# Optimization experiments

Hardware: AMD Instinct MI355X
Metric: run time of the kernel (lower is better)

The kernel has to match this reference:

```python
import jax, jax.numpy as jnp
import numpy as np

DIM = 512
NUM_HEADS = 4  # min(4, 512 // 16)
HEAD_DIM = DIM // NUM_HEADS  # 128


def setup_inputs() -> dict:
    key = jax.random.key(0)
    ks = jax.random.split(key, 5)
    B, N = 2, 4096
    s = DIM ** -0.5
    return {
        "x": jax.random.normal(ks[0], (B, N, DIM), dtype=jnp.float32),
        "qkv_w": jax.random.normal(ks[1], (3 * DIM, DIM), dtype=jnp.float32) * s,
        "qkv_b": jax.random.normal(ks[2], (3 * DIM,), dtype=jnp.float32) * 0.02,
        "proj_w": jax.random.normal(ks[3], (DIM, DIM), dtype=jnp.float32) * s,
        "proj_b": jax.random.normal(ks[4], (DIM,), dtype=jnp.float32) * 0.02,
    }


def reference(x, qkv_w, qkv_b, proj_w, proj_b):
    B, N, C = x.shape
    H, D = NUM_HEADS, HEAD_DIM
    # torch Linear: x @ W^T + b
    qkv = x @ qkv_w.T + qkv_b                      # [B, N, 3C]
    qkv = qkv.reshape(B, N, 3, H, D)
    q = qkv[:, :, 0].transpose(0, 2, 1, 3)         # [B, H, N, D]
    k = qkv[:, :, 1].transpose(0, 2, 1, 3)
    v = qkv[:, :, 2].transpose(0, 2, 1, 3)
    scale = D ** -0.5
    attn = jnp.einsum('bhnd,bhmd->bhnm', q, k) * scale  # [B, H, N, N]
    attn = jax.nn.softmax(attn, axis=-1)
    # dropout(p=0.1) is identity in eval mode
    out = jnp.einsum('bhnm,bhmd->bhnd', attn, v)   # [B, H, N, D]
    out = out.transpose(0, 2, 1, 3).reshape(B, N, C)
    return out @ proj_w.T + proj_b
```

## Files before the change

### kernel.cpp

```cpp
#include <hip/hip_runtime.h>
#include <hip/hip_bf16.h>
#include <stdint.h>

constexpr int B_  = 2;
constexpr int N_  = 4096;
constexpr int C_  = 512;
constexpr int H_  = 4;
constexpr int D_  = 128;
constexpr int M_  = B_ * N_;
constexpr int TC_ = 3 * C_;
constexpr float SCALE_  = 0.08838834764831845f;
constexpr float LOG2E_  = 1.4426950408889634f;
constexpr float KSCALE_ = SCALE_ * LOG2E_;

typedef __attribute__((ext_vector_type(8))) short short8;
typedef __attribute__((ext_vector_type(4))) float f32x4;

#define GLOBAL_AS __attribute__((address_space(1)))
#define LDS_AS    __attribute__((address_space(3)))

static __device__ __forceinline__ void load_lds16(const void* gp, void* lp) {
    __builtin_amdgcn_global_load_lds((const GLOBAL_AS void*)gp, (LDS_AS void*)lp,
                                     16, 0, 0);
}

static __device__ __forceinline__ uint16_t f2bf(float f) {
    uint32_t u = __builtin_bit_cast(uint32_t, f);
    uint32_t r = (u + 0x7FFFu + ((u >> 16) & 1u)) >> 16;
    return (uint16_t)r;
}
static __device__ __forceinline__ uint32_t cvt_pk_bf16(float lo, float hi) {
    uint32_t r;
    asm("v_cvt_pk_bf16_f32 %0, %1, %2" : "=v"(r) : "v"(lo), "v"(hi));
    return r;
}
static __device__ __forceinline__ float exp2f_fast(float x) {
    float r;
    asm("v_exp_f32 %0, %1" : "=v"(r) : "v"(x));
    return r;
}

__global__ __launch_bounds__(256)
void cast3_kernel(const float* __restrict__ x,  const float* __restrict__ w,
                  const float* __restrict__ pw,
                  uint16_t* __restrict__ xb, uint16_t* __restrict__ wb,
                  uint16_t* __restrict__ pwb)
{
    const int bid = blockIdx.x;
    const float* src; uint16_t* dst; int i;
    if (bid < 2048)      { src = x;  dst = xb;  i = bid * 256 + threadIdx.x; }
    else if (bid < 2432) { src = w;  dst = wb;  i = (bid - 2048) * 256 + threadIdx.x; }
    else                 { src = pw; dst = pwb; i = (bid - 2432) * 256 + threadIdx.x; }
    float4 a = reinterpret_cast<const float4*>(src)[2*i];
    float4 b = reinterpret_cast<const float4*>(src)[2*i+1];
    uint4 o;
    o.x = (uint32_t)f2bf(a.x) | ((uint32_t)f2bf(a.y) << 16);
    o.y = (uint32_t)f2bf(a.z) | ((uint32_t)f2bf(a.w) << 16);
    o.z = (uint32_t)f2bf(b.x) | ((uint32_t)f2bf(b.y) << 16);
    o.w = (uint32_t)f2bf(b.z) | ((uint32_t)f2bf(b.w) << 16);
    reinterpret_cast<uint4*>(dst)[i] = o;
}

__global__ __launch_bounds__(256, 2)
void gemm_qkv(const uint16_t* __restrict__ A,
              const uint16_t* __restrict__ Bw,
              const float* __restrict__ bias,
              uint16_t* __restrict__ Qb,
              uint16_t* __restrict__ Kb,
              uint16_t* __restrict__ Vt)
{
    __shared__ __align__(16) uint16_t SMEM[128 * 128];
    uint16_t* As = SMEM;
    uint16_t* Bs = SMEM + 128 * 64;

    const int tid  = threadIdx.x;
    const int lane = tid & 63;
    const int w    = tid >> 6;
    const int wr   = w >> 1, wc = w & 1;
    const int cq   = lane & 15;
    const int g    = lane >> 4;
    const int m0   = blockIdx.x * 128;
    const int o0   = blockIdx.y * 128;

    f32x4 acc[4][4];
    const f32x4 zf = {0.f, 0.f, 0.f, 0.f};
    #pragma unroll
    for (int i = 0; i < 4; ++i)
        #pragma unroll
        for (int j = 0; j < 4; ++j) acc[i][j] = zf;

    for (int kt = 0; kt < C_; kt += 64) {
        __syncthreads();
        #pragma unroll
        for (int i = 0; i < 4; ++i) {
            int s = tid + 256 * i;
            int row = s >> 3, p = s & 7, c = p ^ (row & 7);
            load_lds16(A  + (size_t)(m0 + row) * C_ + kt + c * 8, &As[row*64 + p*8]);
            load_lds16(Bw + (size_t)(o0 + row) * C_ + kt + c * 8, &Bs[row*64 + p*8]);
        }
        __syncthreads();
        #pragma unroll
        for (int ks = 0; ks < 2; ++ks) {
            short8 af[4], bfr[4];
            #pragma unroll
            for (int mi = 0; mi < 4; ++mi) {
                int r = 64*wr + 16*mi + cq;
                af[mi] = *reinterpret_cast<const short8*>(
                    &As[r*64 + (((g + 4*ks) ^ (r & 7)) * 8)]);
            }
            #pragma unroll
            for (int ni = 0; ni < 4; ++ni) {
                int r = 64*wc + 16*ni + cq;
                bfr[ni] = *reinterpret_cast<const short8*>(
                    &Bs[r*64 + (((g + 4*ks) ^ (r & 7)) * 8)]);
            }
            #pragma unroll
            for (int mi = 0; mi < 4; ++mi)
                #pragma unroll
                for (int ni = 0; ni < 4; ++ni)
                    acc[mi][ni] = __builtin_amdgcn_mfma_f32_16x16x32_bf16(
                        af[mi], bfr[ni], acc[mi][ni], 0, 0, 0);
        }
    }

    const int sec = o0 >> 9;
    const int h   = (o0 >> 7) & 3;
    if (sec < 2) {
        #pragma unroll
        for (int ni = 0; ni < 4; ++ni) {
            const int o = o0 + 64*wc + 16*ni + cq;
            const int d = o & 127;
            const float bv = bias[o];
            #pragma unroll
            for (int mi = 0; mi < 4; ++mi) {
                #pragma unroll
                for (int r = 0; r < 4; ++r) {
                    const int m = m0 + 64*wr + 16*mi + 4*g + r;
                    const int b = m >> 12;
                    const int n = m & (N_ - 1);
                    const float y = acc[mi][ni][r] + bv;
                    if (sec == 0)
                        Qb[(((size_t)b*H_ + h)*N_ + n)*D_ + d] = f2bf(y);
                    else
                        Kb[(((size_t)b*H_ + h)*N_ + n)*D_ + d] = f2bf(y * KSCALE_);
                }
            }
        }
    } else {
        __syncthreads();
        uint16_t* T = SMEM;
        #pragma unroll
        for (int ni = 0; ni < 4; ++ni) {
            const int ol = 64*wc + 16*ni + cq;
            const float bv = bias[o0 + ol];
            #pragma unroll
            for (int mi = 0; mi < 4; ++mi) {
                const int ml = 64*wr + 16*mi + 4*g;
                const uint32_t w0 = (uint32_t)f2bf(acc[mi][ni][0] + bv)
                                  | ((uint32_t)f2bf(acc[mi][ni][1] + bv) << 16);
                const uint32_t w1 = (uint32_t)f2bf(acc[mi][ni][2] + bv)
                                  | ((uint32_t)f2bf(acc[mi][ni][3] + bv) << 16);
                *reinterpret_cast<uint2*>(&T[ol*128 + ml]) = make_uint2(w0, w1);
            }
        }
        __syncthreads();
        const int b = m0 >> 12;
        #pragma unroll
        for (int i = 0; i < 8; ++i) {
            int s = tid + 256 * i;
            int ro = s >> 4, mc = s & 15;
            int4 v = *reinterpret_cast<const int4*>(&T[ro*128 + mc*8]);
            const int n = (m0 & (N_ - 1)) + mc*8;
            *reinterpret_cast<int4*>(
                &Vt[(((size_t)b*H_ + h)*D_ + ro)*N_ + n]) = v;
        }
    }
}

__global__ __launch_bounds__(512, 1)
void attn_kernel(const uint16_t* __restrict__ Qb,
                 const uint16_t* __restrict__ Kb,
                 const uint16_t* __restrict__ Vt,
                 uint16_t* __restrict__ ctx)
{
    __shared__ __align__(16) uint16_t Ks[2][128 * 128];
    __shared__ __align__(16) uint16_t Vs[2][128 * 128];
    __shared__ __align__(16) uint16_t Ps[8][16 * 80];

    const int tid  = threadIdx.x;
    const int lane = tid & 63;
    const int w    = tid >> 6;
    const int qb   = w & 3;
    const int kvh  = w >> 2;
    const int cq   = lane & 15;
    const int g    = lane >> 4;

    const int bid = blockIdx.x;
    const int bh  = bid & 7;
    const int qt  = bid >> 3;
    const int b   = bh >> 2, h = bh & 3;

    const uint16_t* Qg = Qb + ((size_t)bh * N_ + qt * 128 + qb * 32) * D_;
    const uint16_t* Kg = Kb + (size_t)bh * N_ * D_;
    const uint16_t* Vg = Vt + (size_t)bh * D_ * N_;

    auto stage = [&](int tn, int bb) {
        const int kv0 = tn * 128;
        #pragma unroll
        for (int i = 0; i < 4; ++i) {
            int s = tid + 512 * i;
            int row = s >> 4, p = s & 15, c = p ^ (row & 15);
            load_lds16(Kg + (size_t)(kv0 + row) * D_ + c * 8,
                       &Ks[bb][row * 128 + p * 8]);
        }
        #pragma unroll
        for (int i = 0; i < 4; ++i) {
            int s = tid + 512 * i;
            int row = s >> 4, p = s & 15, c = p ^ (row & 15);
            load_lds16(Vg + (size_t)row * N_ + kv0 + c * 8,
                       &Vs[bb][row * 128 + p * 8]);
        }
    };

    stage(0, 0);

    short8 qreg[2][4];
    #pragma unroll
    for (int qf = 0; qf < 2; ++qf) {
        const uint16_t* qrow = Qg + (size_t)(16 * qf + cq) * D_;
        #pragma unroll
        for (int ks = 0; ks < 4; ++ks)
            qreg[qf][ks] = *reinterpret_cast<const short8*>(qrow + 32*ks + 8*g);
    }

    float m_run[2] = {-3.0e38f, -3.0e38f};
    float l_run[2] = {0.f, 0.f};
    f32x4 o_acc[8][2];
    const f32x4 zf = {0.f, 0.f, 0.f, 0.f};
    #pragma unroll
    for (int df = 0; df < 8; ++df) { o_acc[df][0] = zf; o_acc[df][1] = zf; }

    __syncthreads();

    for (int t = 0; t < N_ / 128; ++t) {
        const int cur = t & 1;
        if (t + 1 < N_ / 128) stage(t + 1, cur ^ 1);

        f32x4 sacc[4][2];
        #pragma unroll
        for (int kvf = 0; kvf < 4; ++kvf) { sacc[kvf][0] = zf; sacc[kvf][1] = zf; }
        #pragma unroll
        for (int ks = 0; ks < 4; ++ks) {
            #pragma unroll
            for (int kvf = 0; kvf < 4; ++kvf) {
                const int row = kvh*64 + 16*kvf + cq;
                const short8 ak = *reinterpret_cast<const short8*>(
                    &Ks[cur][row * 128 + (((g + 4*ks) ^ (row & 15)) * 8)]);
                sacc[kvf][0] = __builtin_amdgcn_mfma_f32_16x16x32_bf16(
                    ak, qreg[0][ks], sacc[kvf][0], 0, 0, 0);
                sacc[kvf][1] = __builtin_amdgcn_mfma_f32_16x16x32_bf16(
                    ak, qreg[1][ks], sacc[kvf][1], 0, 0, 0);
            }
        }

        short8 bp[2][2];
        #pragma unroll
        for (int qf = 0; qf < 2; ++qf) {
            float pmax = -3.0e38f;
            #pragma unroll
            for (int kvf = 0; kvf < 4; ++kvf)
                #pragma unroll
                for (int r = 0; r < 4; ++r)
                    pmax = fmaxf(pmax, sacc[kvf][qf][r]);
            pmax = fmaxf(pmax, __shfl_xor(pmax, 16));
            pmax = fmaxf(pmax, __shfl_xor(pmax, 32));

            if (__any(pmax > m_run[qf] + 8.f)) {
                const float mnew = fmaxf(m_run[qf], pmax);
                const float corr = exp2f_fast(m_run[qf] - mnew);
                m_run[qf] = mnew;
                l_run[qf] *= corr;
                #pragma unroll
                for (int df = 0; df < 8; ++df)
                    #pragma unroll
                    for (int r = 0; r < 4; ++r)
                        o_acc[df][qf][r] *= corr;
            }

            float lsum = 0.f;
            #pragma unroll
            for (int kvf = 0; kvf < 4; ++kvf) {
                const float p0 = exp2f_fast(sacc[kvf][qf][0] - m_run[qf]);
                const float p1 = exp2f_fast(sacc[kvf][qf][1] - m_run[qf]);
                const float p2 = exp2f_fast(sacc[kvf][qf][2] - m_run[qf]);
                const float p3 = exp2f_fast(sacc[kvf][qf][3] - m_run[qf]);
                lsum += (p0 + p1) + (p2 + p3);
                *reinterpret_cast<uint2*>(&Ps[w][cq*80 + 16*kvf + 4*g]) =
                    make_uint2(cvt_pk_bf16(p0, p1), cvt_pk_bf16(p2, p3));
            }
            lsum += __shfl_xor(lsum, 16);
            lsum += __shfl_xor(lsum, 32);
            l_run[qf] += lsum;

            #pragma unroll
            for (int ks = 0; ks < 2; ++ks)
                bp[qf][ks] = *reinterpret_cast<const short8*>(
                    &Ps[w][cq*80 + (4*ks + g) * 8]);
        }

        #pragma unroll
        for (int ks = 0; ks < 2; ++ks) {
            #pragma unroll
            for (int df = 0; df < 8; ++df) {
                const int row = 16*df + cq;
                const int ch  = kvh*8 + 4*ks + g;
                const short8 av = *reinterpret_cast<const short8*>(
                    &Vs[cur][row * 128 + ((ch ^ (row & 15)) * 8)]);
                o_acc[df][0] = __builtin_amdgcn_mfma_f32_16x16x32_bf16(
                    av, bp[0][ks], o_acc[df][0], 0, 0, 0);
                o_acc[df][1] = __builtin_amdgcn_mfma_f32_16x16x32_bf16(
                    av, bp[1][ks], o_acc[df][1], 0, 0, 0);
            }
        }
        __syncthreads();
    }

    float* mbuf = reinterpret_cast<float*>(&Ks[0][0]);
    float* lbuf = mbuf + 256;
    f32x4* obuf = reinterpret_cast<f32x4*>(&Vs[0][0]);

    if (kvh == 1) {
        #pragma unroll
        for (int qf = 0; qf < 2; ++qf) {
            mbuf[(qb*2 + qf)*16 + cq] = m_run[qf];
            lbuf[(qb*2 + qf)*16 + cq] = l_run[qf];
        }
        #pragma unroll
        for (int df = 0; df < 8; ++df)
            #pragma unroll
            for (int qf = 0; qf < 2; ++qf)
                obuf[qb*1024 + (df*2 + qf)*64 + lane] = o_acc[df][qf];
    }
    __syncthreads();
    if (kvh == 0) {
        #pragma unroll
        for (int qf = 0; qf < 2; ++qf) {
            const float mB = mbuf[(qb*2 + qf)*16 + cq];
            const float lB = lbuf[(qb*2 + qf)*16 + cq];
            const float ms = fmaxf(m_run[qf], mB);
            const float cA = exp2f_fast(m_run[qf] - ms);
            const float cB = exp2f_fast(mB - ms);
            const float inv = 1.f / (l_run[qf] * cA + lB * cB);

            const int n = qt*128 + qb*32 + 16*qf + cq;
            uint16_t* dst = ctx + ((size_t)b * N_ + n) * C_ + h * D_;
            #pragma unroll
            for (int df = 0; df < 8; ++df) {
                const f32x4 oB = obuf[qb*1024 + (df*2 + qf)*64 + lane];
                float v0 = (o_acc[df][qf][0]*cA + oB[0]*cB) * inv;
                float v1 = (o_acc[df][qf][1]*cA + oB[1]*cB) * inv;
                float v2 = (o_acc[df][qf][2]*cA + oB[2]*cB) * inv;
                float v3 = (o_acc[df][qf][3]*cA + oB[3]*cB) * inv;
                const uint32_t w0 = (uint32_t)f2bf(v0) | ((uint32_t)f2bf(v1) << 16);
                const uint32_t w1 = (uint32_t)f2bf(v2) | ((uint32_t)f2bf(v3) << 16);
                *reinterpret_cast<uint2*>(&dst[16*df + 4*g]) = make_uint2(w0, w1);
            }
        }
    }
}

__global__ __launch_bounds__(256, 2)
void gemm_proj(const uint16_t* __restrict__ A,
               const uint16_t* __restrict__ Bw,
               const float* __restrict__ bias,
               float* __restrict__ out)
{
    __shared__ __align__(16) uint16_t As[128 * 64];
    __shared__ __align__(16) uint16_t Bs[128 * 64];

    const int tid  = threadIdx.x;
    const int lane = tid & 63;
    const int w    = tid >> 6;
    const int wr   = w >> 1, wc = w & 1;
    const int cq   = lane & 15;
    const int g    = lane >> 4;
    const int m0   = blockIdx.x * 128;
    const int o0   = blockIdx.y * 128;

    f32x4 acc[4][4];
    const f32x4 zf = {0.f, 0.f, 0.f, 0.f};
    #pragma unroll
    for (int i = 0; i < 4; ++i)
        #pragma unroll
        for (int j = 0; j < 4; ++j) acc[i][j] = zf;

    for (int kt = 0; kt < C_; kt += 64) {
        __syncthreads();
        #pragma unroll
        for (int i = 0; i < 4; ++i) {
            int s = tid + 256 * i;
            int row = s >> 3, p = s & 7, c = p ^ (row & 7);
            load_lds16(A  + (size_t)(m0 + row) * C_ + kt + c * 8, &As[row*64 + p*8]);
            load_lds16(Bw + (size_t)(o0 + row) * C_ + kt + c * 8, &Bs[row*64 + p*8]);
        }
        __syncthreads();
        #pragma unroll
        for (int ks = 0; ks < 2; ++ks) {
            short8 af[4], bfr[4];
            #pragma unroll
            for (int mi = 0; mi < 4; ++mi) {
                int r = 64*wr + 16*mi + cq;
                af[mi] = *reinterpret_cast<const short8*>(
                    &As[r*64 + (((g + 4*ks) ^ (r & 7)) * 8)]);
            }
            #pragma unroll
            for (int ni = 0; ni < 4; ++ni) {
                int r = 64*wc + 16*ni + cq;
                bfr[ni] = *reinterpret_cast<const short8*>(
                    &Bs[r*64 + (((g + 4*ks) ^ (r & 7)) * 8)]);
            }
            #pragma unroll
            for (int mi = 0; mi < 4; ++mi)
                #pragma unroll
                for (int ni = 0; ni < 4; ++ni)
                    acc[mi][ni] = __builtin_amdgcn_mfma_f32_16x16x32_bf16(
                        af[mi], bfr[ni], acc[mi][ni], 0, 0, 0);
        }
    }

    #pragma unroll
    for (int ni = 0; ni < 4; ++ni) {
        const int o = o0 + 64*wc + 16*ni + cq;
        const float bv = bias[o];
        #pragma unroll
        for (int mi = 0; mi < 4; ++mi) {
            #pragma unroll
            for (int r = 0; r < 4; ++r) {
                const int m = m0 + 64*wr + 16*mi + 4*g + r;
                out[(size_t)m * C_ + o] = acc[mi][ni][r] + bv;
            }
        }
    }
}

extern "C" void kernel_launch(void* const* d_in, const int* in_sizes, int n_in,
                              void* d_out, int out_size, void* d_ws, size_t ws_size,
                              hipStream_t stream)
{
    const float* x      = (const float*)d_in[0];
    const float* qkv_w  = (const float*)d_in[1];
    const float* qkv_b  = (const float*)d_in[2];
    const float* proj_w = (const float*)d_in[3];
    const float* proj_b = (const float*)d_in[4];
    float* out = (float*)d_out;

    uint16_t* xb  = (uint16_t*)d_ws;
    uint16_t* wb  = xb  + (size_t)M_ * C_;
    uint16_t* pwb = wb  + (size_t)TC_ * C_;
    uint16_t* Qb  = pwb + (size_t)C_ * C_;
    uint16_t* Kb  = Qb  + (size_t)B_ * H_ * N_ * D_;
    uint16_t* Vt  = Kb  + (size_t)B_ * H_ * N_ * D_;
    uint16_t* ctx = Vt  + (size_t)B_ * H_ * N_ * D_;

    cast3_kernel<<<2560, 256, 0, stream>>>(x, qkv_w, proj_w, xb, wb, pwb);
    gemm_qkv<<<dim3(M_/128, TC_/128), 256, 0, stream>>>(xb, wb, qkv_b, Qb, Kb, Vt);
    attn_kernel<<<(N_/128) * (B_*H_), 512, 0, stream>>>(Qb, Kb, Vt, ctx);
    gemm_proj<<<dim3(M_/128, C_/128), 256, 0, stream>>>(ctx, pwb, proj_b, out);
}
```

Measured before the change: 196.0 us.

## Halve attention tile sizes to raise occupancy and flatten GEMM grids

The attention kernel now processes 64 queries per block (16 per wave) and 64-key tiles instead of 128, which halves LDS use and per-wave accumulator registers and raises the launch bound to 4 blocks per CU. The grid doubles to 512 blocks, giving more parallelism across CUs, and the P and V LDS swizzles are reworked for the narrower tiles. The QKV and projection GEMMs switch to a 1D grid with explicit tile decoding. The trade-off is less Q reuse of each K/V tile, so twice the K/V traffic per query and more loop iterations with barrier overhead.

```diff
diff --git a/kernel.cpp b/kernel.cpp
--- a/kernel.cpp
+++ b/kernel.cpp
@@ -79,8 +79,9 @@
     const int wr   = w >> 1, wc = w & 1;
     const int cq   = lane & 15;
     const int g    = lane >> 4;
-    const int m0   = blockIdx.x * 128;
-    const int o0   = blockIdx.y * 128;
+    const int bid  = blockIdx.x;
+    const int m0   = (bid & 63) << 7;
+    const int o0   = (bid >> 6) << 7;
 
     f32x4 acc[4][4];
     const f32x4 zf = {0.f, 0.f, 0.f, 0.f};
@@ -177,15 +178,15 @@
     }
 }
 
-__global__ __launch_bounds__(512, 1)
+__global__ __launch_bounds__(512, 4)
 void attn_kernel(const uint16_t* __restrict__ Qb,
                  const uint16_t* __restrict__ Kb,
                  const uint16_t* __restrict__ Vt,
                  uint16_t* __restrict__ ctx)
 {
-    __shared__ __align__(16) uint16_t Ks[2][128 * 128];
-    __shared__ __align__(16) uint16_t Vs[2][128 * 128];
-    __shared__ __align__(16) uint16_t Ps[8][16 * 80];
+    __shared__ __align__(16) uint16_t Ks[2][64 * 128];
+    __shared__ __align__(16) uint16_t Vs[2][128 * 64];
+    __shared__ __align__(16) uint16_t Ps[8 * 512];
 
     const int tid  = threadIdx.x;
     const int lane = tid & 63;
@@ -200,171 +201,148 @@
     const int qt  = bid >> 3;
     const int b   = bh >> 2, h = bh & 3;
 
-    const uint16_t* Qg = Qb + ((size_t)bh * N_ + qt * 128 + qb * 32) * D_;
+    const uint16_t* Qg = Qb + ((size_t)bh * N_ + qt * 64 + qb * 16) * D_;
     const uint16_t* Kg = Kb + (size_t)bh * N_ * D_;
     const uint16_t* Vg = Vt + (size_t)bh * D_ * N_;
 
     auto stage = [&](int tn, int bb) {
-        const int kv0 = tn * 128;
-        #pragma unroll
-        for (int i = 0; i < 4; ++i) {
+        const int kv0 = tn * 64;
+        #pragma unroll
+        for (int i = 0; i < 2; ++i) {
             int s = tid + 512 * i;
             int row = s >> 4, p = s & 15, c = p ^ (row & 15);
             load_lds16(Kg + (size_t)(kv0 + row) * D_ + c * 8,
                        &Ks[bb][row * 128 + p * 8]);
         }
         #pragma unroll
-        for (int i = 0; i < 4; ++i) {
+        for (int i = 0; i < 2; ++i) {
             int s = tid + 512 * i;
-            int row = s >> 4, p = s & 15, c = p ^ (row & 15);
+            int row = s >> 3, p = s & 7, c = p ^ (row & 7);
             load_lds16(Vg + (size_t)row * N_ + kv0 + c * 8,
-                       &Vs[bb][row * 128 + p * 8]);
+                       &Vs[bb][row * 64 + p * 8]);
         }
     };
 
     stage(0, 0);
 
-    short8 qreg[2][4];
-    #pragma unroll
-    for (int qf = 0; qf < 2; ++qf) {
-        const uint16_t* qrow = Qg + (size_t)(16 * qf + cq) * D_;
+    short8 qreg[4];
+    {
+        const uint16_t* qrow = Qg + (size_t)cq * D_;
         #pragma unroll
         for (int ks = 0; ks < 4; ++ks)
-            qreg[qf][ks] = *reinterpret_cast<const short8*>(qrow + 32*ks + 8*g);
-    }
-
-    float m_run[2] = {-3.0e38f, -3.0e38f};
-    float l_run[2] = {0.f, 0.f};
-    f32x4 o_acc[8][2];
+            qreg[ks] = *reinterpret_cast<const short8*>(qrow + 32*ks + 8*g);
+    }
+
+    float m_run = -3.0e38f, l_run = 0.f;
+    f32x4 o_acc[8];
     const f32x4 zf = {0.f, 0.f, 0.f, 0.f};
     #pragma unroll
-    for (int df = 0; df < 8; ++df) { o_acc[df][0] = zf; o_acc[df][1] = zf; }
+    for (int df = 0; df < 8; ++df) o_acc[df] = zf;
 
     __syncthreads();
 
-    for (int t = 0; t < N_ / 128; ++t) {
+    for (int t = 0; t < N_ / 64; ++t) {
         const int cur = t & 1;
-        if (t + 1 < N_ / 128) stage(t + 1, cur ^ 1);
-
-        f32x4 sacc[4][2];
-        #pragma unroll
-        for (int kvf = 0; kvf < 4; ++kvf) { sacc[kvf][0] = zf; sacc[kvf][1] = zf; }
+        if (t + 1 < N_ / 64) stage(t + 1, cur ^ 1);
+
+        f32x4 sacc[2];
+        sacc[0] = zf; sacc[1] = zf;
         #pragma unroll
         for (int ks = 0; ks < 4; ++ks) {
             #pragma unroll
-            for (int kvf = 0; kvf < 4; ++kvf) {
-                const int row = kvh*64 + 16*kvf + cq;
+            for (int kvf = 0; kvf < 2; ++kvf) {
+                const int row = kvh*32 + 16*kvf + cq;
                 const short8 ak = *reinterpret_cast<const short8*>(
-                    &Ks[cur][row * 128 + (((g + 4*ks) ^ (row & 15)) * 8)]);
-                sacc[kvf][0] = __builtin_amdgcn_mfma_f32_16x16x32_bf16(
-                    ak, qreg[0][ks], sacc[kvf][0], 0, 0, 0);
-                sacc[kvf][1] = __builtin_amdgcn_mfma_f32_16x16x32_bf16(
-                    ak, qreg[1][ks], sacc[kvf][1], 0, 0, 0);
-            }
-        }
-
-        short8 bp[2][2];
-        #pragma unroll
-        for (int qf = 0; qf < 2; ++qf) {
-            float pmax = -3.0e38f;
-            #pragma unroll
-            for (int kvf = 0; kvf < 4; ++kvf)
+                    &Ks[cur][row * 128 + (((g + 4*ks) ^ cq) * 8)]);
+                sacc[kvf] = __builtin_amdgcn_mfma_f32_16x16x32_bf16(
+                    ak, qreg[ks], sacc[kvf], 0, 0, 0);
+            }
+        }
+
+        float pmax = -3.0e38f;
+        #pragma unroll
+        for (int kvf = 0; kvf < 2; ++kvf)
+            #pragma unroll
+            for (int r = 0; r < 4; ++r)
+                pmax = fmaxf(pmax, sacc[kvf][r]);
+        pmax = fmaxf(pmax, __shfl_xor(pmax, 16));
+        pmax = fmaxf(pmax, __shfl_xor(pmax, 32));
+
+        if (__any(pmax > m_run + 8.f)) {
+            const float mnew = fmaxf(m_run, pmax);
+            const float corr = exp2f_fast(m_run - mnew);
+            m_run = mnew;
+            l_run *= corr;
+            #pragma unroll
+            for (int df = 0; df < 8; ++df)
                 #pragma unroll
                 for (int r = 0; r < 4; ++r)
-                    pmax = fmaxf(pmax, sacc[kvf][qf][r]);
-            pmax = fmaxf(pmax, __shfl_xor(pmax, 16));
-            pmax = fmaxf(pmax, __shfl_xor(pmax, 32));
-
-            if (__any(pmax > m_run[qf] + 8.f)) {
-                const float mnew = fmaxf(m_run[qf], pmax);
-                const float corr = exp2f_fast(m_run[qf] - mnew);
-                m_run[qf] = mnew;
-                l_run[qf] *= corr;
-                #pragma unroll
-                for (int df = 0; df < 8; ++df)
-                    #pragma unroll
-                    for (int r = 0; r < 4; ++r)
-                        o_acc[df][qf][r] *= corr;
-            }
-
-            float lsum = 0.f;
-            #pragma unroll
-            for (int kvf = 0; kvf < 4; ++kvf) {
-                const float p0 = exp2f_fast(sacc[kvf][qf][0] - m_run[qf]);
-                const float p1 = exp2f_fast(sacc[kvf][qf][1] - m_run[qf]);
-                const float p2 = exp2f_fast(sacc[kvf][qf][2] - m_run[qf]);
-                const float p3 = exp2f_fast(sacc[kvf][qf][3] - m_run[qf]);
-                lsum += (p0 + p1) + (p2 + p3);
-                *reinterpret_cast<uint2*>(&Ps[w][cq*80 + 16*kvf + 4*g]) =
-                    make_uint2(cvt_pk_bf16(p0, p1), cvt_pk_bf16(p2, p3));
-            }
-            lsum += __shfl_xor(lsum, 16);
-            lsum += __shfl_xor(lsum, 32);
-            l_run[qf] += lsum;
-
-            #pragma unroll
-            for (int ks = 0; ks < 2; ++ks)
-                bp[qf][ks] = *reinterpret_cast<const short8*>(
-                    &Ps[w][cq*80 + (4*ks + g) * 8]);
-        }
-
-        #pragma unroll
-        for (int ks = 0; ks < 2; ++ks) {
-            #pragma unroll
-            for (int df = 0; df < 8; ++df) {
-                const int row = 16*df + cq;
-                const int ch  = kvh*8 + 4*ks + g;
-                const short8 av = *reinterpret_cast<const short8*>(
-                    &Vs[cur][row * 128 + ((ch ^ (row & 15)) * 8)]);
-                o_acc[df][0] = __builtin_amdgcn_mfma_f32_16x16x32_bf16(
-                    av, bp[0][ks], o_acc[df][0], 0, 0, 0);
-                o_acc[df][1] = __builtin_amdgcn_mfma_f32_16x16x32_bf16(
-                    av, bp[1][ks], o_acc[df][1], 0, 0, 0);
-            }
-        }
-        __syncthreads();
-    }
-
-    float* mbuf = reinterpret_cast<float*>(&Ks[0][0]);
-    float* lbuf = mbuf + 256;
-    f32x4* obuf = reinterpret_cast<f32x4*>(&Vs[0][0]);
+                    o_acc[df][r] *= corr;
+        }
+
+        float lsum = 0.f;
+        #pragma unroll
+        for (int kvf = 0; kvf < 2; ++kvf) {
+            const float p0 = exp2f_fast(sacc[kvf][0] - m_run);
+            const float p1 = exp2f_fast(sacc[kvf][1] - m_run);
+            const float p2 = exp2f_fast(sacc[kvf][2] - m_run);
+            const float p3 = exp2f_fast(sacc[kvf][3] - m_run);
+            lsum += (p0 + p1) + (p2 + p3);
+            const int c8p = (4*kvf + g) ^ ((cq & 3) << 1);
+            *reinterpret_cast<uint2*>(&Ps[w*512 + cq*32 + c8p*4]) =
+                make_uint2(cvt_pk_bf16(p0, p1), cvt_pk_bf16(p2, p3));
+        }
+        lsum += __shfl_xor(lsum, 16);
+        lsum += __shfl_xor(lsum, 32);
+        l_run += lsum;
+
+        const short8 bp = *reinterpret_cast<const short8*>(
+            &Ps[w*512 + cq*32 + ((g ^ (cq & 3)) << 3)]);
+
+        #pragma unroll
+        for (int df = 0; df < 8; ++df) {
+            const int row = 16*df + cq;
+            const int ch  = (4*kvh + g) ^ (cq & 7);
+            const short8 av = *reinterpret_cast<const short8*>(
+                &Vs[cur][row * 64 + ch * 8]);
+            o_acc[df] = __builtin_amdgcn_mfma_f32_16x16x32_bf16(
+                av, bp, o_acc[df], 0, 0, 0);
+        }
+        __syncthreads();
+    }
+
+    float* mbuf = reinterpret_cast<float*>(&Vs[0][0]);
+    float* lbuf = mbuf + 64;
+    f32x4* obuf = reinterpret_cast<f32x4*>(&Ks[0][0]);
 
     if (kvh == 1) {
-        #pragma unroll
-        for (int qf = 0; qf < 2; ++qf) {
-            mbuf[(qb*2 + qf)*16 + cq] = m_run[qf];
-            lbuf[(qb*2 + qf)*16 + cq] = l_run[qf];
-        }
+        mbuf[qb*16 + cq] = m_run;
+        lbuf[qb*16 + cq] = l_run;
         #pragma unroll
         for (int df = 0; df < 8; ++df)
-            #pragma unroll
-            for (int qf = 0; qf < 2; ++qf)
-                obuf[qb*1024 + (df*2 + qf)*64 + lane] = o_acc[df][qf];
+            obuf[(qb*8 + df)*64 + lane] = o_acc[df];
     }
     __syncthreads();
     if (kvh == 0) {
-        #pragma unroll
-        for (int qf = 0; qf < 2; ++qf) {
-            const float mB = mbuf[(qb*2 + qf)*16 + cq];
-            const float lB = lbuf[(qb*2 + qf)*16 + cq];
-            const float ms = fmaxf(m_run[qf], mB);
-            const float cA = exp2f_fast(m_run[qf] - ms);
-            const float cB = exp2f_fast(mB - ms);
-            const float inv = 1.f / (l_run[qf] * cA + lB * cB);
-
-            const int n = qt*128 + qb*32 + 16*qf + cq;
-            uint16_t* dst = ctx + ((size_t)b * N_ + n) * C_ + h * D_;
-            #pragma unroll
-            for (int df = 0; df < 8; ++df) {
-                const f32x4 oB = obuf[qb*1024 + (df*2 + qf)*64 + lane];
-                float v0 = (o_acc[df][qf][0]*cA + oB[0]*cB) * inv;
-                float v1 = (o_acc[df][qf][1]*cA + oB[1]*cB) * inv;
-                float v2 = (o_acc[df][qf][2]*cA + oB[2]*cB) * inv;
-                float v3 = (o_acc[df][qf][3]*cA + oB[3]*cB) * inv;
-                const uint32_t w0 = (uint32_t)f2bf(v0) | ((uint32_t)f2bf(v1) << 16);
-                const uint32_t w1 = (uint32_t)f2bf(v2) | ((uint32_t)f2bf(v3) << 16);
-                *reinterpret_cast<uint2*>(&dst[16*df + 4*g]) = make_uint2(w0, w1);
-            }
+        const float mB = mbuf[qb*16 + cq];
+        const float lB = lbuf[qb*16 + cq];
+        const float ms = fmaxf(m_run, mB);
+        const float cA = exp2f_fast(m_run - ms);
+        const float cB = exp2f_fast(mB - ms);
+        const float inv = 1.f / (l_run * cA + lB * cB);
+
+        const int n = qt*64 + qb*16 + cq;
+        uint16_t* dst = ctx + ((size_t)b * N_ + n) * C_ + h * D_;
+        #pragma unroll
+        for (int df = 0; df < 8; ++df) {
+            const f32x4 oB = obuf[(qb*8 + df)*64 + lane];
+            float v0 = (o_acc[df][0]*cA + oB[0]*cB) * inv;
+            float v1 = (o_acc[df][1]*cA + oB[1]*cB) * inv;
+            float v2 = (o_acc[df][2]*cA + oB[2]*cB) * inv;
+            float v3 = (o_acc[df][3]*cA + oB[3]*cB) * inv;
+            const uint32_t w0 = (uint32_t)f2bf(v0) | ((uint32_t)f2bf(v1) << 16);
+            const uint32_t w1 = (uint32_t)f2bf(v2) | ((uint32_t)f2bf(v3) << 16);
+            *reinterpret_cast<uint2*>(&dst[16*df + 4*g]) = make_uint2(w0, w1);
         }
     }
 }
@@ -384,8 +362,9 @@
     const int wr   = w >> 1, wc = w & 1;
     const int cq   = lane & 15;
     const int g    = lane >> 4;
-    const int m0   = blockIdx.x * 128;
-    const int o0   = blockIdx.y * 128;
+    const int bid  = blockIdx.x;
+    const int m0   = (bid & 63) << 7;
+    const int o0   = (bid >> 6) << 7;
 
     f32x4 acc[4][4];
     const f32x4 zf = {0.f, 0.f, 0.f, 0.f};
@@ -463,7 +442,7 @@
     uint16_t* ctx = Vt  + (size_t)B_ * H_ * N_ * D_;
 
     cast3_kernel<<<2560, 256, 0, stream>>>(x, qkv_w, proj_w, xb, wb, pwb);
-    gemm_qkv<<<dim3(M_/128, TC_/128), 256, 0, stream>>>(xb, wb, qkv_b, Qb, Kb, Vt);
-    attn_kernel<<<(N_/128) * (B_*H_), 512, 0, stream>>>(Qb, Kb, Vt, ctx);
-    gemm_proj<<<dim3(M_/128, C_/128), 256, 0, stream>>>(ctx, pwb, proj_b, out);
-}
+    gemm_qkv<<<(M_/128) * (TC_/128), 256, 0, stream>>>(xb, wb, qkv_b, Qb, Kb, Vt);
+    attn_kernel<<<(N_/64) * (B_*H_), 512, 0, stream>>>(Qb, Kb, Vt, ctx);
+    gemm_proj<<<(M_/128) * (C_/128), 256, 0, stream>>>(ctx, pwb, proj_b, out);
+}
```

Result: slower. 206.7 us (+5.5%).
